# Performance work log

Hardware: AMD Instinct MI355X
Metric: run time of the kernel (lower is better)

Reference implementation:

```python
import jax, jax.numpy as jnp
import numpy as np

NUM_HEADS = 16

def setup_inputs() -> dict:
    key = jax.random.key(0)
    ks = jax.random.split(key, 5)
    B, S, H = 16, 1025, 1024
    std = 0.02
    return {
        "hidden_states": jax.random.normal(ks[0], (B, S, H), jnp.float32),
        "w_qkv": jax.random.normal(ks[1], (3 * H, H), jnp.float32) * std,
        "b_qkv": jax.random.normal(ks[2], (3 * H,), jnp.float32) * std,
        "w_dense": jax.random.normal(ks[3], (H, H), jnp.float32) * std,
        "b_dense": jax.random.normal(ks[4], (H,), jnp.float32) * std,
    }

def reference(hidden_states, w_qkv, b_qkv, w_dense, b_dense):
    B, S, H = hidden_states.shape
    nh = NUM_HEADS
    hd = H // nh
    scale = hd ** -0.5
    # fused QKV projection: [B,S,3H]
    mixed = jnp.einsum('bsh,oh->bso', hidden_states, w_qkv) + b_qkv
    # reshape per torch: (B,S,nh,3,hd) -> permute(3,0,2,1,4)
    mixed = mixed.reshape(B, S, nh, 3, hd).transpose(3, 0, 2, 1, 4)
    q, k, v = mixed[0], mixed[1], mixed[2]          # each [B,nh,S,hd]
    scores = jnp.einsum('bhqd,bhkd->bhqk', q, k) * scale
    probs = jax.nn.softmax(scores, axis=-1)          # [B,nh,S,S]
    ctx = jnp.einsum('bhqk,bhkd->bhqd', probs, v)    # [B,nh,S,hd]
    ctx = ctx.transpose(0, 2, 1, 3).reshape(B, S, H)
    out = jnp.einsum('bsh,oh->bso', ctx, w_dense) + b_dense
    return out
```

## Files before the change

kernel.cpp:

```cpp
#include <hip/hip_runtime.h>
#include <math.h>

typedef float f32x4 __attribute__((ext_vector_type(4)));
typedef __bf16 bf16x8 __attribute__((ext_vector_type(8)));
typedef unsigned int u32;
typedef u32 u32x4 __attribute__((ext_vector_type(4)));

#define AS1 __attribute__((address_space(1)))
#define AS3 __attribute__((address_space(3)))

static __device__ __forceinline__ void gload16(const void* g, void* l) {
    __builtin_amdgcn_global_load_lds((const AS1 u32*)g, (AS3 u32*)l, 16, 0, 0);
}
static __device__ __forceinline__ f32x4 mfma16(bf16x8 a, bf16x8 b, f32x4 c) {
    return __builtin_amdgcn_mfma_f32_16x16x32_bf16(a, b, c, 0, 0, 0);
}
static __device__ __forceinline__ float exp2fast(float x) {
    return __builtin_amdgcn_exp2f(x);
}

__global__ __launch_bounds__(256)
void convert3_kernel(const float* __restrict__ in0, __bf16* __restrict__ out0, int nb0,
                     const float* __restrict__ in1, __bf16* __restrict__ out1, int nb1,
                     const float* __restrict__ in2, __bf16* __restrict__ out2)
{
    int b = blockIdx.x;
    const float* in; __bf16* out;
    if (b < nb0)            { in = in0; out = out0; }
    else if (b < nb0 + nb1) { in = in1; out = out1; b -= nb0; }
    else                    { in = in2; out = out2; b -= nb0 + nb1; }
    const size_t i = ((size_t)b * 256 + threadIdx.x) * 8;
    f32x4 a = *(const f32x4*)(in + i);
    f32x4 c = *(const f32x4*)(in + i + 4);
    bf16x8 o;
    #pragma unroll
    for (int j = 0; j < 4; ++j) { o[j] = (__bf16)a[j]; o[j + 4] = (__bf16)c[j]; }
    *(bf16x8*)(out + i) = o;
}

template<int MODE>
__global__ __launch_bounds__(512)
void gemm_big(const __bf16* __restrict__ A, const __bf16* __restrict__ Bw,
              const float* __restrict__ bias, __bf16* __restrict__ qkv,
              float* __restrict__ f_out)
{
    constexpr int M = 16400;
    constexpr int K = 1024;
    constexpr int NBX = (MODE == 0) ? 24 : 8;
    constexpr int NOUT = (MODE == 0) ? 3072 : 1024;
    constexpr int CHUNK = (65 * NBX) / 8;

    __shared__ __align__(16) __bf16 As[256 * 64];
    __shared__ __align__(16) __bf16 Bs[128 * 64];

    const int tid  = threadIdx.x;
    const int lane = tid & 63;
    const int wv   = tid >> 6;
    const int wrm  = wv >> 1;
    const int wcn  = wv & 1;
    const int fr   = lane & 15, fq = lane >> 4;

    const int xx = blockIdx.x & 7, jj = blockIdx.x >> 3;
    const int tile = xx * CHUNK + jj;
    const int by = tile / NBX, bx = tile % NBX;
    const int m0 = by * 256, n0 = bx * 128;

    const __bf16* aptr[4]; int aoff[4];
    #pragma unroll
    for (int qd = 0; qd < 4; ++qd) {
        const int s = qd * 512 + tid;
        const int r = s >> 3;
        const int c = (s & 7) ^ (r & 7);
        aoff[qd] = s * 8;
        int ar = m0 + r; if (ar > M - 1) ar = M - 1;
        aptr[qd] = A + (size_t)ar * K + c * 8;
    }
    const __bf16* bptr[2]; int boff[2];
    #pragma unroll
    for (int l = 0; l < 2; ++l) {
        const int s = l * 512 + tid;
        const int r = s >> 3;
        const int c = (s & 7) ^ (r & 7);
        boff[l] = s * 8;
        bptr[l] = Bw + (size_t)(n0 + r) * K + c * 8;
    }

    f32x4 acc[4][4];
    #pragma unroll
    for (int i = 0; i < 4; ++i)
        #pragma unroll
        for (int j = 0; j < 4; ++j)
            acc[i][j] = f32x4{0.f, 0.f, 0.f, 0.f};

    for (int kt = 0; kt < K / 64; ++kt) {
        const int kof = kt * 64;
        #pragma unroll
        for (int qd = 0; qd < 4; ++qd) gload16(aptr[qd] + kof, &As[aoff[qd]]);
        #pragma unroll
        for (int l = 0; l < 2; ++l)   gload16(bptr[l] + kof, &Bs[boff[l]]);
        __syncthreads();

        #pragma unroll
        for (int ks = 0; ks < 2; ++ks) {
            bf16x8 a[4], b[4];
            #pragma unroll
            for (int i = 0; i < 4; ++i) {
                const int ra = wrm * 64 + i * 16 + fr;
                const int rb = wcn * 64 + i * 16 + fr;
                const int cga = ((ks * 4 + fq) ^ (ra & 7)) * 8;
                const int cgb = ((ks * 4 + fq) ^ (rb & 7)) * 8;
                a[i] = *(const bf16x8*)&As[ra * 64 + cga];
                b[i] = *(const bf16x8*)&Bs[rb * 64 + cgb];
            }
            #pragma unroll
            for (int i = 0; i < 4; ++i)
                #pragma unroll
                for (int j = 0; j < 4; ++j)
                    acc[i][j] = mfma16(a[i], b[j], acc[i][j]);
        }
        __syncthreads();
    }

    #pragma unroll
    for (int ni = 0; ni < 4; ++ni) {
        const int col = n0 + wcn * 64 + ni * 16 + fr;
        const float bv = bias[col];
        if constexpr (MODE == 0) {
            const float scale = ((col % 192) < 64) ? 0.18033688011112042f : 1.0f;
            #pragma unroll
            for (int mi = 0; mi < 4; ++mi) {
                #pragma unroll
                for (int j = 0; j < 4; ++j) {
                    const int m = m0 + wrm * 64 + mi * 16 + fq * 4 + j;
                    if (m < M)
                        qkv[(size_t)m * NOUT + col] =
                            (__bf16)((acc[mi][ni][j] + bv) * scale);
                }
            }
        } else {
            #pragma unroll
            for (int mi = 0; mi < 4; ++mi) {
                #pragma unroll
                for (int j = 0; j < 4; ++j) {
                    const int m = m0 + wrm * 64 + mi * 16 + fq * 4 + j;
                    if (m < M) f_out[(size_t)m * NOUT + col] = acc[mi][ni][j] + bv;
                }
            }
        }
    }
}

__global__ __launch_bounds__(256)
void transpose_v(const __bf16* __restrict__ qkvb, __bf16* __restrict__ vt)
{
    constexpr int S = 1025, S2 = 1088;
    const int bh = blockIdx.y;
    const int bb = bh >> 4, hh = bh & 15;
    const int s0 = blockIdx.x * 64;
    const int sr = threadIdx.x >> 2, sq = threadIdx.x & 3;
    int srow = s0 + sr; if (srow > S - 1) srow = S - 1;
    const __bf16* src = qkvb + ((size_t)(bb * 1025) + srow) * 3072
                             + hh * 192 + 128 + sq * 16;
    bf16x8 v0 = *(const bf16x8*)src;
    bf16x8 v1 = *(const bf16x8*)(src + 8);
    __bf16* dst = vt + (size_t)bh * 64 * S2 + s0 + sr;
    #pragma unroll
    for (int i = 0; i < 8; ++i) {
        dst[(size_t)(sq * 16 + i) * S2]     = v0[i];
        dst[(size_t)(sq * 16 + 8 + i) * S2] = v1[i];
    }
}

__global__ __launch_bounds__(512)
void attn_kernel(const __bf16* __restrict__ qkvb, const __bf16* __restrict__ vtb,
                 __bf16* __restrict__ ctxb)
{
    constexpr int S = 1025, S2 = 1088, ROW = 3072;
    const int tid  = threadIdx.x;
    const int lane = tid & 63;
    const int w    = tid >> 6;
    const int fr   = lane & 15, fq = lane >> 4;

    const int xx = blockIdx.x & 7, jj = blockIdx.x >> 3;
    const int tile = xx * 288 + jj;
    const int bh = tile / 9;
    const int q0 = (tile % 9) * 128;
    const int bb = bh >> 4, hh = bh & 15;

    const __bf16* qp = qkvb + (size_t)(bb * 1025) * ROW + hh * 192;
    const __bf16* kp = qp + 64;
    const __bf16* vp = vtb + (size_t)bh * 64 * S2;

    __shared__ __align__(16) __bf16 Ks[64 * 64];
    __shared__ __align__(16) __bf16 Vs[64 * 64];
    __shared__ u32 Ps[8][16 * 33];

    const int r0 = tid >> 3, g0 = (tid & 7) ^ ((tid >> 3) & 7);

    int qrow = q0 + w * 16 + fr; if (qrow > S - 1) qrow = S - 1;
    const bf16x8 qa0 = *(const bf16x8*)(qp + (size_t)qrow * ROW + fq * 8);
    const bf16x8 qa1 = *(const bf16x8*)(qp + (size_t)qrow * ROW + 32 + fq * 8);

    f32x4 ctx[4];
    #pragma unroll
    for (int di = 0; di < 4; ++di) ctx[di] = f32x4{0.f, 0.f, 0.f, 0.f};
    float mrow = -1e30f;
    float lrow = 0.f;

    u32* psrow_w = &Ps[w][fr * 33];

    for (int kt = 0; kt < 17; ++kt) {
        const int kv0 = kt * 64;
        {
            int kr = kv0 + r0; if (kr > S - 1) kr = S - 1;
            gload16(kp + (size_t)kr * ROW + g0 * 8, &Ks[tid * 8]);
            gload16(vp + (size_t)r0 * S2 + kv0 + g0 * 8, &Vs[tid * 8]);
        }
        __syncthreads();

        f32x4 sc[4];
        #pragma unroll
        for (int ni = 0; ni < 4; ++ni) {
            const int row = ni * 16 + fr;
            bf16x8 kf0 = *(const bf16x8*)&Ks[row * 64 + ((fq    ) ^ (row & 7)) * 8];
            bf16x8 kf1 = *(const bf16x8*)&Ks[row * 64 + ((fq + 4) ^ (row & 7)) * 8];
            f32x4 z = f32x4{0.f, 0.f, 0.f, 0.f};
            z = mfma16(kf0, qa0, z);
            sc[ni] = mfma16(kf1, qa1, z);
        }
        if (kv0 + 64 > S) {
            #pragma unroll
            for (int ni = 0; ni < 4; ++ni)
                #pragma unroll
                for (int j = 0; j < 4; ++j)
                    if (kv0 + ni * 16 + fq * 4 + j >= S) sc[ni][j] = -1e30f;
        }

        float mt = sc[0][0];
        #pragma unroll
        for (int ni = 0; ni < 4; ++ni)
            #pragma unroll
            for (int j = 0; j < 4; ++j) mt = fmaxf(mt, sc[ni][j]);
        mt = fmaxf(mt, __shfl_xor(mt, 16, 64));
        mt = fmaxf(mt, __shfl_xor(mt, 32, 64));

        if (__any(mt > mrow + 8.0f)) {
            const float mnew = fmaxf(mrow, mt);
            const float alpha = exp2fast(mrow - mnew);
            mrow = mnew;
            lrow *= alpha;
            float av[4];
            #pragma unroll
            for (int j = 0; j < 4; ++j) av[j] = __shfl(alpha, fq * 4 + j, 64);
            #pragma unroll
            for (int di = 0; di < 4; ++di) {
                ctx[di][0] *= av[0]; ctx[di][1] *= av[1];
                ctx[di][2] *= av[2]; ctx[di][3] *= av[3];
            }
        }

        float p[4][4];
        float s = 0.f;
        #pragma unroll
        for (int ni = 0; ni < 4; ++ni)
            #pragma unroll
            for (int j = 0; j < 4; ++j) {
                p[ni][j] = exp2fast(sc[ni][j] - mrow);
                s += p[ni][j];
            }
        s += __shfl_xor(s, 16, 64);
        s += __shfl_xor(s, 32, 64);
        lrow += s;

        #pragma unroll
        for (int ni = 0; ni < 4; ++ni) {
            #pragma unroll
            for (int h = 0; h < 2; ++h) {
                unsigned short lo = __builtin_bit_cast(unsigned short, (__bf16)p[ni][2 * h]);
                unsigned short hi = __builtin_bit_cast(unsigned short, (__bf16)p[ni][2 * h + 1]);
                psrow_w[fq * 8 + ni * 2 + h] = (u32)lo | ((u32)hi << 16);
            }
        }
        u32x4 pav[2];
        #pragma unroll
        for (int ks = 0; ks < 2; ++ks)
            #pragma unroll
            for (int t = 0; t < 4; ++t) {
                const int slot = (2 * (fq & 1) + (t >> 1)) * 8
                               + (2 * ks + (fq >> 1)) * 2 + (t & 1);
                pav[ks][t] = psrow_w[slot];
            }

        #pragma unroll
        for (int ks = 0; ks < 2; ++ks) {
            const bf16x8 pa = __builtin_bit_cast(bf16x8, pav[ks]);
            #pragma unroll
            for (int di = 0; di < 4; ++di) {
                const int row = di * 16 + fr;
                bf16x8 vf = *(const bf16x8*)&Vs[row * 64 + ((ks * 4 + fq) ^ (row & 7)) * 8];
                ctx[di] = mfma16(pa, vf, ctx[di]);
            }
        }
        __syncthreads();
    }

    float linv[4];
    #pragma unroll
    for (int j = 0; j < 4; ++j) linv[j] = 1.0f / __shfl(lrow, fq * 4 + j, 64);
    #pragma unroll
    for (int di = 0; di < 4; ++di) {
        #pragma unroll
        for (int j = 0; j < 4; ++j) {
            const int qg = q0 + w * 16 + fq * 4 + j;
            if (qg < S) {
                ctxb[((size_t)bb * 1025 + qg) * 1024 + hh * 64 + di * 16 + fr] =
                    (__bf16)(ctx[di][j] * linv[j]);
            }
        }
    }
}

extern "C" void kernel_launch(void* const* d_in, const int* in_sizes, int n_in,
                              void* d_out, int out_size, void* d_ws, size_t ws_size,
                              hipStream_t stream)
{
    const float* hs      = (const float*)d_in[0];
    const float* w_qkv   = (const float*)d_in[1];
    const float* b_qkv   = (const float*)d_in[2];
    const float* w_dense = (const float*)d_in[3];
    const float* b_dense = (const float*)d_in[4];

    const size_t nHS  = (size_t)16 * 1025 * 1024;
    const size_t nWQ  = (size_t)3072 * 1024;
    const size_t nWD  = (size_t)1024 * 1024;
    const size_t nQKV = (size_t)16400 * 3072;

    __bf16* hsb     = (__bf16*)d_ws;
    __bf16* wqkvb   = hsb + nHS;
    __bf16* wdenseb = wqkvb + nWQ;
    __bf16* qkvb    = wdenseb + nWD;
    __bf16* ctxb    = qkvb + nQKV;
    __bf16* vtb     = ctxb + nHS;

    convert3_kernel<<<dim3(8200 + 1536 + 512), dim3(256), 0, stream>>>(
        hs, hsb, 8200, w_qkv, wqkvb, 1536, w_dense, wdenseb);

    gemm_big<0><<<dim3(65 * 24), dim3(512), 0, stream>>>(
        hsb, wqkvb, b_qkv, qkvb, nullptr);

    transpose_v<<<dim3(17, 256), dim3(256), 0, stream>>>(qkvb, vtb);

    attn_kernel<<<dim3(8 * 288), dim3(512), 0, stream>>>(qkvb, vtb, ctxb);

    gemm_big<1><<<dim3(65 * 8), dim3(512), 0, stream>>>(
        ctxb, wdenseb, b_dense, nullptr, (float*)d_out);
}
```

Baseline: 389.7 us.

## Fuse V transpose into QKV GEMM epilogue and group tiles for L2 reuse

The QKV GEMM epilogue now writes the V slice straight into the transposed per-head layout that attention reads. This removes the separate transpose_v kernel, along with its read-back of V and its rewrite. Q and K still go to the packed buffer, and the V columns of that buffer are no longer written. MODE 0 also remaps block indices into 5x4 supertiles so neighbouring blocks share A and B tiles in L2. The trade-offs: the transposed V stores are scattered 2-byte writes strided by the padded sequence length, and the padding columns past sequence length 1025 are no longer filled with clamped values.

Result: no change. 384.2 us (-1.4%).

```diff
diff --git a/kernel.cpp b/kernel.cpp
--- a/kernel.cpp
+++ b/kernel.cpp
@@ -42,7 +42,7 @@
 __global__ __launch_bounds__(512)
 void gemm_big(const __bf16* __restrict__ A, const __bf16* __restrict__ Bw,
               const float* __restrict__ bias, __bf16* __restrict__ qkv,
-              float* __restrict__ f_out)
+              __bf16* __restrict__ vt, float* __restrict__ f_out)
 {
     constexpr int M = 16400;
     constexpr int K = 1024;
@@ -61,8 +61,15 @@
     const int fr   = lane & 15, fq = lane >> 4;
 
     const int xx = blockIdx.x & 7, jj = blockIdx.x >> 3;
-    const int tile = xx * CHUNK + jj;
-    const int by = tile / NBX, bx = tile % NBX;
+    const int g  = xx * CHUNK + jj;
+    int by, bx;
+    if constexpr (MODE == 0) {
+        const int s = g / 20, r = g % 20;
+        by = (s / 6) * 5 + (r >> 2);
+        bx = (s % 6) * 4 + (r & 3);
+    } else {
+        by = g / NBX; bx = g % NBX;
+    }
     const int m0 = by * 256, n0 = bx * 128;
 
     const __bf16* aptr[4]; int aoff[4];
@@ -107,10 +114,8 @@
             for (int i = 0; i < 4; ++i) {
                 const int ra = wrm * 64 + i * 16 + fr;
                 const int rb = wcn * 64 + i * 16 + fr;
-                const int cga = ((ks * 4 + fq) ^ (ra & 7)) * 8;
-                const int cgb = ((ks * 4 + fq) ^ (rb & 7)) * 8;
-                a[i] = *(const bf16x8*)&As[ra * 64 + cga];
-                b[i] = *(const bf16x8*)&Bs[rb * 64 + cgb];
+                a[i] = *(const bf16x8*)&As[ra * 64 + ((ks * 4 + fq) ^ (ra & 7)) * 8];
+                b[i] = *(const bf16x8*)&Bs[rb * 64 + ((ks * 4 + fq) ^ (rb & 7)) * 8];
             }
             #pragma unroll
             for (int i = 0; i < 4; ++i)
@@ -126,15 +131,34 @@
         const int col = n0 + wcn * 64 + ni * 16 + fr;
         const float bv = bias[col];
         if constexpr (MODE == 0) {
-            const float scale = ((col % 192) < 64) ? 0.18033688011112042f : 1.0f;
-            #pragma unroll
-            for (int mi = 0; mi < 4; ++mi) {
-                #pragma unroll
-                for (int j = 0; j < 4; ++j) {
-                    const int m = m0 + wrm * 64 + mi * 16 + fq * 4 + j;
-                    if (m < M)
-                        qkv[(size_t)m * NOUT + col] =
-                            (__bf16)((acc[mi][ni][j] + bv) * scale);
+            const int tsel = (col >> 6) % 3;
+            if (tsel < 2) {
+                const float scale = (tsel == 0) ? 0.18033688011112042f : 1.0f;
+                #pragma unroll
+                for (int mi = 0; mi < 4; ++mi) {
+                    #pragma unroll
+                    for (int j = 0; j < 4; ++j) {
+                        const int m = m0 + wrm * 64 + mi * 16 + fq * 4 + j;
+                        if (m < M)
+                            qkv[(size_t)m * 3072 + col] =
+                                (__bf16)((acc[mi][ni][j] + bv) * scale);
+                    }
+                }
+            } else {
+                const int head = col / 192;
+                const int d    = col & 63;
+                #pragma unroll
+                for (int mi = 0; mi < 4; ++mi) {
+                    #pragma unroll
+                    for (int j = 0; j < 4; ++j) {
+                        const int m = m0 + wrm * 64 + mi * 16 + fq * 4 + j;
+                        if (m < M) {
+                            const int bb = m / 1025;
+                            const int ss = m - bb * 1025;
+                            vt[((size_t)((bb * 16 + head) * 64 + d)) * 1088 + ss] =
+                                (__bf16)(acc[mi][ni][j] + bv);
+                        }
+                    }
                 }
             }
         } else {
@@ -147,27 +171,6 @@
                 }
             }
         }
-    }
-}
-
-__global__ __launch_bounds__(256)
-void transpose_v(const __bf16* __restrict__ qkvb, __bf16* __restrict__ vt)
-{
-    constexpr int S = 1025, S2 = 1088;
-    const int bh = blockIdx.y;
-    const int bb = bh >> 4, hh = bh & 15;
-    const int s0 = blockIdx.x * 64;
-    const int sr = threadIdx.x >> 2, sq = threadIdx.x & 3;
-    int srow = s0 + sr; if (srow > S - 1) srow = S - 1;
-    const __bf16* src = qkvb + ((size_t)(bb * 1025) + srow) * 3072
-                             + hh * 192 + 128 + sq * 16;
-    bf16x8 v0 = *(const bf16x8*)src;
-    bf16x8 v1 = *(const bf16x8*)(src + 8);
-    __bf16* dst = vt + (size_t)bh * 64 * S2 + s0 + sr;
-    #pragma unroll
-    for (int i = 0; i < 8; ++i) {
-        dst[(size_t)(sq * 16 + i) * S2]     = v0[i];
-        dst[(size_t)(sq * 16 + 8 + i) * S2] = v1[i];
     }
 }
 
@@ -346,12 +349,10 @@
         hs, hsb, 8200, w_qkv, wqkvb, 1536, w_dense, wdenseb);
 
     gemm_big<0><<<dim3(65 * 24), dim3(512), 0, stream>>>(
-        hsb, wqkvb, b_qkv, qkvb, nullptr);
-
-    transpose_v<<<dim3(17, 256), dim3(256), 0, stream>>>(qkvb, vtb);
+        hsb, wqkvb, b_qkv, qkvb, vtb, nullptr);
 
     attn_kernel<<<dim3(8 * 288), dim3(512), 0, stream>>>(qkvb, vtb, ctxb);
 
     gemm_big<1><<<dim3(65 * 8), dim3(512), 0, stream>>>(
-        ctxb, wdenseb, b_dense, nullptr, (float*)d_out);
-}
+        ctxb, wdenseb, b_dense, nullptr, nullptr, (float*)d_out);
+}
```
